# Kernel tuning notes

Hardware: AMD Instinct MI355X
Metric: run time of the kernel (lower is better)

## Reference

```python
import jax, jax.numpy as jnp
import numpy as np

N = 50000
E = 800000
IN_DIM = 128
HID = 128
OUT_DIM = 128
H = 16
D = OUT_DIM // H  # head_dim = 8
EF = 4
RF = 20
KV_IN = 2 * IN_DIM + EF + RF  # 280
EPS = 1e-5


def _layernorm(x, w, b):
    mu = jnp.mean(x, axis=-1, keepdims=True)
    var = jnp.var(x, axis=-1, keepdims=True)
    return (x - mu) * jax.lax.rsqrt(var + EPS) * w + b


def _mlp(x, W1, b1, ln_w, ln_b, W2, b2):
    # Linear -> LayerNorm -> ReLU -> Linear (num_layer=2, norm=True)
    hdn = x @ W1 + b1
    hdn = jax.nn.relu(_layernorm(hdn, ln_w, ln_b))
    return hdn @ W2 + b2


def _lin_init(key, fan_in, fan_out):
    k1, k2 = jax.random.split(key)
    s = 1.0 / np.sqrt(fan_in)
    W = jax.random.uniform(k1, (fan_in, fan_out), jnp.float32, -s, s)
    b = jax.random.uniform(k2, (fan_out,), jnp.float32, -s, s)
    return W, b


def _mlp_params(key, in_dim, hid, out_dim):
    k1, k2 = jax.random.split(key)
    W1, b1 = _lin_init(k1, in_dim, hid)
    W2, b2 = _lin_init(k2, hid, out_dim)
    return W1, b1, jnp.ones((hid,), jnp.float32), jnp.zeros((hid,), jnp.float32), W2, b2


def setup_inputs() -> dict:
    key = jax.random.key(0)
    ks = jax.random.split(key, 10)
    h = jax.random.normal(ks[0], (N, IN_DIM), jnp.float32)
    rel_x = jax.random.normal(ks[1], (E, 3), jnp.float32)
    r_feat = jax.random.normal(ks[2], (E, RF), jnp.float32)
    edge_feat = jax.random.normal(ks[3], (E, EF), jnp.float32)
    edge_index = jax.random.randint(ks[4], (2, E), 0, N, jnp.int64)

    xk = _mlp_params(ks[5], KV_IN, HID, OUT_DIM)
    xv = _mlp_params(ks[6], KV_IN, HID, H)
    xq = _mlp_params(ks[7], IN_DIM, HID, OUT_DIM)
    ew_W, ew_b = _lin_init(ks[8], RF, 1)

    d = {"h": h, "rel_x": rel_x, "r_feat": r_feat, "edge_feat": edge_feat,
         "edge_index": edge_index, "ew_W": ew_W, "ew_b": ew_b}
    for name, p in (("xk", xk), ("xv", xv), ("xq", xq)):
        d[name + "_W1"], d[name + "_b1"], d[name + "_ln_w"], d[name + "_ln_b"], d[name + "_W2"], d[name + "_b2"] = p
    return d


def reference(h, rel_x, r_feat, edge_feat, edge_index,
              ew_W, ew_b,
              xk_W1, xk_b1, xk_ln_w, xk_ln_b, xk_W2, xk_b2,
              xv_W1, xv_b1, xv_ln_w, xv_ln_b, xv_W2, xv_b2,
              xq_W1, xq_b1, xq_ln_w, xq_ln_b, xq_W2, xq_b2):
    src, dst = edge_index[0], edge_index[1]
    hi = h[dst]  # [E, IN_DIM]
    hj = h[src]  # [E, IN_DIM]
    kv_input = jnp.concatenate([edge_feat, r_feat, hi, hj], axis=-1)  # [E, KV_IN]

    k = _mlp(kv_input, xk_W1, xk_b1, xk_ln_w, xk_ln_b, xk_W2, xk_b2).reshape(E, H, D)
    v = _mlp(kv_input, xv_W1, xv_b1, xv_ln_w, xv_ln_b, xv_W2, xv_b2)  # [E, H]
    e_w = jax.nn.sigmoid(r_feat @ ew_W + ew_b)  # [E, 1]
    v = (v * e_w)[:, :, None] * rel_x[:, None, :]  # [E, H, 3]

    q = _mlp(h, xq_W1, xq_b1, xq_ln_w, xq_ln_b, xq_W2, xq_b2).reshape(N, H, D)
    scores = jnp.sum(q[dst] * k, axis=-1) / np.sqrt(D)  # [E, H]

    # scatter_softmax over destination groups
    seg_max = jax.ops.segment_max(scores, dst, num_segments=N)  # [N, H]
    ex = jnp.exp(scores - seg_max[dst])
    denom = jax.ops.segment_sum(ex, dst, num_segments=N)  # [N, H]
    alpha = ex / denom[dst]  # [E, H]

    m = alpha[:, :, None] * v  # [E, H, 3]
    output = jax.ops.segment_sum(m, dst, num_segments=N)  # [N, H, 3]
    return output.mean(axis=1)  # [N, 3]
```

## Files before the change

### kernel.cpp

```cpp
#include <hip/hip_runtime.h>
#include <hip/hip_bf16.h>

#define NN 50000
#define EE 800000
#define ET 32
#define SCB 49

typedef unsigned int u32;
typedef __attribute__((ext_vector_type(8))) short short8;
typedef __attribute__((ext_vector_type(4))) float floatx4;

template<bool BF>
__device__ __forceinline__ float ldf(const void* p, int i){
  if constexpr (BF) return __bfloat162float(((const __hip_bfloat16*)p)[i]);
  else              return ((const float*)p)[i];
}
__device__ __forceinline__ int gidx(const int* ei, int pos, bool i64){
  return i64 ? ei[2*pos] : ei[pos];
}

__device__ __forceinline__ unsigned short f2bf(float f){
  u32 u = __float_as_uint(f);
  u32 r = u + 0x7FFFu + ((u>>16)&1u);
  return (unsigned short)(r>>16);
}
__device__ __forceinline__ float bf2f(unsigned short s){
  return __uint_as_float(((u32)s)<<16);
}

__global__ void k_detect(const u32* lnw, const u32* ei, int* flags){
  if (threadIdx.x == 0){
    flags[0] = (lnw[0] == 0x3F803F80u) ? 1 : 0;
    flags[1] = ((ei[1] | ei[3] | ei[5] | ei[7]) == 0u) ? 1 : 0;
  }
}

__global__ void __launch_bounds__(256)
k_hist(const int* ei, int* cnt, const int* flags){
  int t = blockIdx.x*256 + threadIdx.x;
  if (t >= EE) return;
  bool i64 = flags[1] != 0;
  atomicAdd(&cnt[gidx(ei, EE + t, i64)], 1);
}

__global__ void __launch_bounds__(256)
k_scan1(const int* cnt, int* bsum){
  __shared__ int wsum[4];
  int t=threadIdx.x, lane=t&63, wv=t>>6;
  int i0 = blockIdx.x*1024 + t*4;
  int s=0;
  #pragma unroll
  for(int j=0;j<4;j++){ int i=i0+j; s += (i<NN)?cnt[i]:0; }
  #pragma unroll
  for(int d=1;d<64;d<<=1) s += __shfl_xor(s,d);
  if(lane==0) wsum[wv]=s;
  __syncthreads();
  if(t==0) bsum[blockIdx.x]=wsum[0]+wsum[1]+wsum[2]+wsum[3];
}

__global__ void k_scan2(const int* bsum, int* bexcl, int* off){
  int lane=threadIdx.x;
  int v = (lane<SCB)?bsum[lane]:0;
  int sc=v;
  #pragma unroll
  for(int d=1;d<64;d<<=1){ int u=__shfl_up(sc,d); if(lane>=d) sc+=u; }
  if(lane<SCB) bexcl[lane]=sc-v;
  if(lane==63) off[NN]=sc;
}

__global__ void __launch_bounds__(256)
k_scan3(const int* cnt, const int* bexcl, int* off){
  __shared__ int wsum[4];
  int t=threadIdx.x, lane=t&63, wv=t>>6;
  int i0=blockIdx.x*1024 + t*4;
  int v0=(i0+0<NN)?cnt[i0+0]:0;
  int v1=(i0+1<NN)?cnt[i0+1]:0;
  int v2=(i0+2<NN)?cnt[i0+2]:0;
  int v3=(i0+3<NN)?cnt[i0+3]:0;
  int s=v0+v1+v2+v3;
  int sc=s;
  #pragma unroll
  for(int d=1;d<64;d<<=1){ int u=__shfl_up(sc,d); if(lane>=d) sc+=u; }
  if(lane==63) wsum[wv]=sc;
  __syncthreads();
  int base=bexcl[blockIdx.x];
  for(int k=0;k<wv;k++) base+=wsum[k];
  int excl=base+sc-s;
  if(i0+0<NN) off[i0+0]=excl;
  if(i0+1<NN) off[i0+1]=excl+v0;
  if(i0+2<NN) off[i0+2]=excl+v0+v1;
  if(i0+3<NN) off[i0+3]=excl+v0+v1+v2;
}

template<bool BF>
__device__ void scat_body(const int* ei, bool i64, const int* off, int* cur,
                          const void* rfeat, const void* relx,
                          const void* ewW, const void* ewb,
                          int* dsts, int* srcs, int* eperm,
                          float* relx_s, float* ews){
  int t = blockIdx.x*256 + threadIdx.x;
  if (t >= EE) return;
  int d = gidx(ei, EE + t, i64);
  int pos = off[d] + atomicAdd(&cur[d], 1);
  dsts[pos] = d;
  srcs[pos] = gidx(ei, t, i64);
  eperm[pos] = t;
  float aw = ldf<BF>(ewb, 0);
  #pragma unroll
  for (int j=0;j<20;j++) aw = fmaf(ldf<BF>(rfeat, t*20+j), ldf<BF>(ewW,j), aw);
  ews[pos] = (1.f/(1.f + expf(-aw))) * (1.f/16.f);
  relx_s[pos*3+0] = ldf<BF>(relx, t*3+0);
  relx_s[pos*3+1] = ldf<BF>(relx, t*3+1);
  relx_s[pos*3+2] = ldf<BF>(relx, t*3+2);
}
__global__ void __launch_bounds__(256)
k_scat(const int* ei, const int* off, int* cur,
       const void* rfeat, const void* relx, const void* ewW, const void* ewb,
       int* dsts, int* srcs, int* eperm, float* relx_s, float* ews, const int* flags){
  bool i64 = flags[1] != 0;
  if (flags[0]) scat_body<true >(ei,i64,off,cur,rfeat,relx,ewW,ewb,dsts,srcs,eperm,relx_s,ews);
  else          scat_body<false>(ei,i64,off,cur,rfeat,relx,ewW,ewb,dsts,srcs,eperm,relx_s,ews);
}

__global__ void __launch_bounds__(256)
k_wprep(const void* kW1, const void* vW1, const void* kW2, const void* vW2,
        const void* qW1, const void* qW2,
        unsigned short* w1sh, unsigned short* w1sl,
        unsigned short* w1nh, unsigned short* w1nl,
        unsigned short* w2kh, unsigned short* w2kl,
        unsigned short* w2vh, unsigned short* w2vl,
        unsigned short* w1qh, unsigned short* w1ql,
        unsigned short* w2qh, unsigned short* w2ql, const int* flags){
  int idx = blockIdx.x*256 + threadIdx.x;
  bool bf = flags[0] != 0;
  {
    int c = idx>>7, k = idx&127;
    int row = (c<256) ? (24+k) : (152+k);
    int cc  = c & 127;
    const void* W = ((c&255)<128) ? kW1 : vW1;
    float f = bf ? __bfloat162float(((const __hip_bfloat16*)W)[row*128+cc]) : ((const float*)W)[row*128+cc];
    unsigned short h = f2bf(f); w1nh[idx]=h; w1nl[idx]=f2bf(f - bf2f(h));
  }
  if (idx < 16384){ int c = idx>>7, k = idx&127;
    { float f = bf ? __bfloat162float(((const __hip_bfloat16*)kW2)[k*128+c]) : ((const float*)kW2)[k*128+c];
      unsigned short h = f2bf(f); w2kh[idx]=h; w2kl[idx]=f2bf(f - bf2f(h)); }
    { float f = bf ? __bfloat162float(((const __hip_bfloat16*)qW1)[k*128+c]) : ((const float*)qW1)[k*128+c];
      unsigned short h = f2bf(f); w1qh[idx]=h; w1ql[idx]=f2bf(f - bf2f(h)); }
    { float f = bf ? __bfloat162float(((const __hip_bfloat16*)qW2)[k*128+c]) : ((const float*)qW2)[k*128+c];
      unsigned short h = f2bf(f); w2qh[idx]=h; w2ql[idx]=f2bf(f - bf2f(h)); }
  }
  if (idx < 2048){ int c = idx>>7, k = idx&127;
    float f = bf ? __bfloat162float(((const __hip_bfloat16*)vW2)[k*16+c]) : ((const float*)vW2)[k*16+c];
    unsigned short h = f2bf(f); w2vh[idx]=h; w2vl[idx]=f2bf(f - bf2f(h)); }
  if (idx < 8192){ int c = idx>>5, k = idx&31;
    float f = 0.f;
    if (k < 24){
      if (c < 128) f = bf ? __bfloat162float(((const __hip_bfloat16*)kW1)[k*128+c]) : ((const float*)kW1)[k*128+c];
      else         f = bf ? __bfloat162float(((const __hip_bfloat16*)vW1)[k*128+(c-128)]) : ((const float*)vW1)[k*128+(c-128)];
    }
    unsigned short h = f2bf(f); w1sh[idx]=h; w1sl[idx]=f2bf(f - bf2f(h)); }
}

template<bool BF>
__device__ void nodeq_body(const void* h,
                           const unsigned short* w1nh, const unsigned short* w1nl,
                           const unsigned short* w1qh, const unsigned short* w1ql,
                           const unsigned short* w2qh, const unsigned short* w2ql,
                           const void* qb1, const void* qlnw, const void* qlnb, const void* qb2,
                           float* hkd, float* hks, float* qws,
                           unsigned short* xh, unsigned short* xl,
                           unsigned short* yh, unsigned short* yl,
                           float2 (*lnred)[4]){
  const int t = threadIdx.x;
  const int n0 = blockIdx.x*16;
  const int lane = t&63, w = t>>6;
  const int arow = lane&15, agrp = lane>>4;
  { int nd = t>>4, c8 = (t&15)*8;
    float v[8];
    if constexpr (!BF){
      float4 a = *(const float4*)&((const float*)h)[(n0+nd)*128 + c8];
      float4 b = *(const float4*)&((const float*)h)[(n0+nd)*128 + c8 + 4];
      v[0]=a.x; v[1]=a.y; v[2]=a.z; v[3]=a.w; v[4]=b.x; v[5]=b.y; v[6]=b.z; v[7]=b.w;
    } else {
      short8 raw = *(const short8*)&((const __hip_bfloat16*)h)[(n0+nd)*128 + c8];
      #pragma unroll
      for (int i=0;i<8;i++) v[i] = bf2f((unsigned short)raw[i]);
    }
    short8 hv, lv;
    #pragma unroll
    for (int i=0;i<8;i++){
      unsigned short hh = f2bf(v[i]);
      hv[i] = (short)hh; lv[i] = (short)f2bf(v[i]-bf2f(hh));
    }
    int sidx = (nd*128 + c8) ^ ((nd&7)<<3);
    *(short8*)&xh[sidx] = hv;
    *(short8*)&xl[sidx] = lv;
  }
  __syncthreads();
  { floatx4 acc[8];
    #pragma unroll
    for (int ct=0; ct<8; ct++)
      #pragma unroll
      for (int r=0;r<4;r++) acc[ct][r]=0.f;
    #pragma unroll
    for (int ks=0; ks<4; ks++){
      int aidx = (arow*128 + ks*32 + agrp*8) ^ ((arow&7)<<3);
      short8 Ah = *(const short8*)&xh[aidx];
      short8 Al = *(const short8*)&xl[aidx];
      #pragma unroll
      for (int ct=0; ct<8; ct++){
        int gc = w*128 + ct*16 + arow;
        short8 Bh = *(const short8*)&w1nh[gc*128 + ks*32 + agrp*8];
        short8 Bl = *(const short8*)&w1nl[gc*128 + ks*32 + agrp*8];
        acc[ct] = __builtin_amdgcn_mfma_f32_16x16x32_bf16(Ah, Bh, acc[ct], 0,0,0);
        acc[ct] = __builtin_amdgcn_mfma_f32_16x16x32_bf16(Al, Bh, acc[ct], 0,0,0);
        acc[ct] = __builtin_amdgcn_mfma_f32_16x16x32_bf16(Ah, Bl, acc[ct], 0,0,0);
      }
    }
    #pragma unroll
    for (int ct=0; ct<8; ct++){
      int gc = w*128 + ct*16 + arow;
      float* dst = (gc<256) ? (hkd + (size_t)0) : (hks - 256);
      #pragma unroll
      for (int r=0;r<4;r++){
        int n = n0 + agrp*4 + r;
        dst[(size_t)n*256 + gc] = acc[ct][r];
      }
    }
  }
  floatx4 Cq[2];
  #pragma unroll
  for (int nt=0; nt<2; nt++){
    int col = w*32 + nt*16 + arow;
    float bb = ldf<BF>(qb1, col);
    #pragma unroll
    for (int r=0;r<4;r++) Cq[nt][r] = bb;
  }
  #pragma unroll
  for (int ks=0; ks<4; ks++){
    int aidx = (arow*128 + ks*32 + agrp*8) ^ ((arow&7)<<3);
    short8 Ah = *(const short8*)&xh[aidx];
    short8 Al = *(const short8*)&xl[aidx];
    #pragma unroll
    for (int nt=0; nt<2; nt++){
      int col = w*32 + nt*16 + arow;
      short8 Bh = *(const short8*)&w1qh[col*128 + ks*32 + agrp*8];
      short8 Bl = *(const short8*)&w1ql[col*128 + ks*32 + agrp*8];
      Cq[nt] = __builtin_amdgcn_mfma_f32_16x16x32_bf16(Ah, Bh, Cq[nt], 0,0,0);
      Cq[nt] = __builtin_amdgcn_mfma_f32_16x16x32_bf16(Al, Bh, Cq[nt], 0,0,0);
      Cq[nt] = __builtin_amdgcn_mfma_f32_16x16x32_bf16(Ah, Bl, Cq[nt], 0,0,0);
    }
  }
  { float s1[4], s2[4];
    #pragma unroll
    for (int r=0;r<4;r++){ s1[r]=0.f; s2[r]=0.f; }
    #pragma unroll
    for (int nt=0; nt<2; nt++)
      #pragma unroll
      for (int r=0;r<4;r++){ float v=Cq[nt][r]; s1[r]+=v; s2[r]=fmaf(v,v,s2[r]); }
    #pragma unroll
    for (int d=1; d<16; d<<=1){
      #pragma unroll
      for (int r=0;r<4;r++){ s1[r]+=__shfl_xor(s1[r],d); s2[r]+=__shfl_xor(s2[r],d); }
    }
    if (arow==0){
      #pragma unroll
      for (int r=0;r<4;r++) lnred[agrp*4+r][w] = make_float2(s1[r], s2[r]);
    }
  }
  __syncthreads();
  float mu[4], rs[4];
  #pragma unroll
  for (int r=0;r<4;r++){
    int row = agrp*4+r;
    float s=0.f, q=0.f;
    #pragma unroll
    for (int k=0;k<4;k++){ float2 p=lnred[row][k]; s+=p.x; q+=p.y; }
    float m = s*(1.f/128.f);
    mu[r]=m; rs[r]=rsqrtf(q*(1.f/128.f) - m*m + 1e-5f);
  }
  #pragma unroll
  for (int nt=0; nt<2; nt++){
    int col = w*32 + nt*16 + arow;
    float lw = ldf<BF>(qlnw, col), lb = ldf<BF>(qlnb, col);
    #pragma unroll
    for (int r=0;r<4;r++){
      int row = agrp*4+r;
      float v = fmaxf((Cq[nt][r]-mu[r])*rs[r]*lw + lb, 0.f);
      unsigned short hh = f2bf(v);
      int idx = (row*128 + col) ^ ((row&7)<<3);
      yh[idx] = hh;
      yl[idx] = f2bf(v - bf2f(hh));
    }
  }
  __syncthreads();
  floatx4 Co[2];
  #pragma unroll
  for (int nt=0; nt<2; nt++){
    int col = w*32 + nt*16 + arow;
    float bb = ldf<BF>(qb2, col);
    #pragma unroll
    for (int r=0;r<4;r++) Co[nt][r] = bb;
  }
  #pragma unroll
  for (int ks=0; ks<4; ks++){
    int aidx = (arow*128 + ks*32 + agrp*8) ^ ((arow&7)<<3);
    short8 Ah = *(const short8*)&yh[aidx];
    short8 Al = *(const short8*)&yl[aidx];
    #pragma unroll
    for (int nt=0; nt<2; nt++){
      int col = w*32 + nt*16 + arow;
      short8 Bh = *(const short8*)&w2qh[col*128 + ks*32 + agrp*8];
      short8 Bl = *(const short8*)&w2ql[col*128 + ks*32 + agrp*8];
      Co[nt] = __builtin_amdgcn_mfma_f32_16x16x32_bf16(Ah, Bh, Co[nt], 0,0,0);
      Co[nt] = __builtin_amdgcn_mfma_f32_16x16x32_bf16(Al, Bh, Co[nt], 0,0,0);
      Co[nt] = __builtin_amdgcn_mfma_f32_16x16x32_bf16(Ah, Bl, Co[nt], 0,0,0);
    }
  }
  #pragma unroll
  for (int nt=0; nt<2; nt++){
    int col = w*32 + nt*16 + arow;
    #pragma unroll
    for (int r=0;r<4;r++){
      int n = n0 + agrp*4 + r;
      qws[(size_t)n*128 + col] = Co[nt][r];
    }
  }
}
__global__ void __launch_bounds__(256)
k_nodeq(const void* h,
        const unsigned short* w1nh, const unsigned short* w1nl,
        const unsigned short* w1qh, const unsigned short* w1ql,
        const unsigned short* w2qh, const unsigned short* w2ql,
        const void* qb1, const void* qlnw, const void* qlnb, const void* qb2,
        float* hkd, float* hks, float* qws, const int* flags){
  __shared__ unsigned short xh[16*128];
  __shared__ unsigned short xl[16*128];
  __shared__ unsigned short yh[16*128];
  __shared__ unsigned short yl[16*128];
  __shared__ float2 lnred[16][4];
  if (flags[0]) nodeq_body<true >(h,w1nh,w1nl,w1qh,w1ql,w2qh,w2ql,qb1,qlnw,qlnb,qb2,hkd,hks,qws,xh,xl,yh,yl,lnred);
  else          nodeq_body<false>(h,w1nh,w1nl,w1qh,w1ql,w2qh,w2ql,qb1,qlnw,qlnb,qb2,hkd,hks,qws,xh,xl,yh,yl,lnred);
}

template<bool BF>
__device__ void edge_body(const void* rfeat, const void* efeat,
                          const int* dsts, const int* srcs, const int* eperm,
                          const void* kb1, const void* vb1,
                          const void* klnw, const void* klnb,
                          const void* vlnw, const void* vlnb,
                          const void* kb2, const void* vb2,
                          const unsigned short* w1sh, const unsigned short* w1sl,
                          const unsigned short* w2kh, const unsigned short* w2kl,
                          const unsigned short* w2vh, const unsigned short* w2vl,
                          const float* hkd, const float* hks, const float* qws,
                          const float* ews, float* scw, float* vsw,
                          unsigned short* ahi, unsigned short* sfh,
                          int* dste, int* srce, float* ewv,
                          float2 (*lnred)[4], float* sc_lds){
  const int t  = threadIdx.x;
  const int e0 = blockIdx.x*ET;
  const int lane = t&63, w = t>>6;
  const int arow = lane&15, agrp = lane>>4;

  if (t < ET)             dste[t]    = dsts[e0+t];
  else if (t < 2*ET)      srce[t-ET] = srcs[e0+(t-ET)];
  else if (t < 3*ET)      ewv[t-2*ET] = ews[e0+(t-2*ET)];
  #pragma unroll
  for (int it=0; it<4; it++){
    int id = it*256+t; int e = id>>5, j = id&31;
    int ge = eperm[e0+e];
    float f = (j<4) ? ldf<BF>(efeat, ge*4+j)
            : (j<24 ? ldf<BF>(rfeat, ge*20+(j-4)) : 0.f);
    sfh[e*40+j] = f2bf(f);
  }
  __syncthreads();

  const int wcol = w*64 + arow;
  float b1c[4];
  #pragma unroll
  for (int nt=0; nt<4; nt++){ int col = wcol + nt*16;
    b1c[nt] = (col<128) ? ldf<BF>(kb1,col) : ldf<BF>(vb1,col-128); }
  floatx4 C[2][4];
  #pragma unroll
  for (int g=0; g<2; g++){
    #pragma unroll
    for (int r=0;r<4;r++){
      int e = g*16 + agrp*4 + r;
      const float* bd = hkd + (u32)dste[e]*256u + wcol;
      const float* bs = hks + (u32)srce[e]*256u + wcol;
      #pragma unroll
      for (int nt=0; nt<4; nt++)
        C[g][nt][r] = bd[nt*16] + bs[nt*16] + b1c[nt];
    }
  }
  #pragma unroll
  for (int g=0; g<2; g++){
    short8 Ah = *(const short8*)&sfh[(g*16+arow)*40 + agrp*8];
    #pragma unroll
    for (int nt=0; nt<4; nt++){
      const int col = wcol + nt*16;
      short8 Bh = *(const short8*)&w1sh[col*32 + agrp*8];
      short8 Bl = *(const short8*)&w1sl[col*32 + agrp*8];
      C[g][nt] = __builtin_amdgcn_mfma_f32_16x16x32_bf16(Ah, Bh, C[g][nt], 0,0,0);
      C[g][nt] = __builtin_amdgcn_mfma_f32_16x16x32_bf16(Ah, Bl, C[g][nt], 0,0,0);
    }
  }
  #pragma unroll
  for (int g=0; g<2; g++){
    float s1[4], s2[4];
    #pragma unroll
    for (int r=0;r<4;r++){ s1[r]=0.f; s2[r]=0.f; }
    #pragma unroll
    for (int nt=0; nt<4; nt++)
      #pragma unroll
      for (int r=0;r<4;r++){ float v=C[g][nt][r]; s1[r]+=v; s2[r]=fmaf(v,v,s2[r]); }
    #pragma unroll
    for (int d=1; d<16; d<<=1){
      #pragma unroll
      for (int r=0;r<4;r++){ s1[r]+=__shfl_xor(s1[r],d); s2[r]+=__shfl_xor(s2[r],d); }
    }
    if (arow==0){
      #pragma unroll
      for (int r=0;r<4;r++) lnred[g*16+agrp*4+r][w] = make_float2(s1[r], s2[r]);
    }
  }
  __syncthreads();
  float mu[2][4], rs[2][4];
  { int b = w>>1;
    #pragma unroll
    for (int g=0; g<2; g++)
      #pragma unroll
      for (int r=0;r<4;r++){
        int row = g*16+agrp*4+r;
        float2 p0 = lnred[row][2*b], p1 = lnred[row][2*b+1];
        float s = p0.x+p1.x, q = p0.y+p1.y;
        float m = s*(1.f/128.f);
        mu[g][r]=m; rs[g][r]=rsqrtf(q*(1.f/128.f) - m*m + 1e-5f);
      }
  }
  #pragma unroll
  for (int nt=0; nt<4; nt++){
    const int col = wcol + nt*16;
    const bool kb = (col<128); const int cc = kb?col:col-128;
    float lw = kb?ldf<BF>(klnw,cc):ldf<BF>(vlnw,cc);
    float lb = kb?ldf<BF>(klnb,cc):ldf<BF>(vlnb,cc);
    #pragma unroll
    for (int g=0; g<2; g++){
      #pragma unroll
      for (int r=0;r<4;r++){
        int row = g*16+agrp*4+r;
        float v = (C[g][nt][r]-mu[g][r])*rs[g][r]*lw + lb;
        v = fmaxf(v, 0.f);
        int idx = (row*256 + col) ^ ((row&7)<<3);
        ahi[idx] = f2bf(v);
      }
    }
  }
  __syncthreads();

  const int c0 = (2*w+0)*16 + arow;
  const int c1 = (2*w+1)*16 + arow;
  floatx4 Ck[2][2], Cv;
  { float b0=ldf<BF>(kb2,c0), b1v=ldf<BF>(kb2,c1);
    #pragma unroll
    for (int g=0;g<2;g++)
      #pragma unroll
      for (int r=0;r<4;r++){ Ck[g][0][r]=b0; Ck[g][1][r]=b1v; } }
  const bool dov = (w&1);
  const int  gv  = w>>1;
  if (dov){ float bv=ldf<BF>(vb2,arow);
    #pragma unroll
    for (int r=0;r<4;r++) Cv[r]=bv; }
  #pragma unroll
  for (int ks=0; ks<4; ks++){
    short8 B0h = *(const short8*)&w2kh[c0*128 + ks*32 + agrp*8];
    short8 B0l = *(const short8*)&w2kl[c0*128 + ks*32 + agrp*8];
    short8 B1h = *(const short8*)&w2kh[c1*128 + ks*32 + agrp*8];
    short8 B1l = *(const short8*)&w2kl[c1*128 + ks*32 + agrp*8];
    #pragma unroll
    for (int g=0; g<2; g++){
      int aidx = ((g*16+arow)*256 + ks*32 + agrp*8) ^ ((arow&7)<<3);
      short8 Ah = *(const short8*)&ahi[aidx];
      Ck[g][0] = __builtin_amdgcn_mfma_f32_16x16x32_bf16(Ah, B0h, Ck[g][0], 0,0,0);
      Ck[g][0] = __builtin_amdgcn_mfma_f32_16x16x32_bf16(Ah, B0l, Ck[g][0], 0,0,0);
      Ck[g][1] = __builtin_amdgcn_mfma_f32_16x16x32_bf16(Ah, B1h, Ck[g][1], 0,0,0);
      Ck[g][1] = __builtin_amdgcn_mfma_f32_16x16x32_bf16(Ah, B1l, Ck[g][1], 0,0,0);
    }
    if (dov){
      int avidx = ((gv*16+arow)*256 + 128 + ks*32 + agrp*8) ^ ((arow&7)<<3);
      short8 Avh = *(const short8*)&ahi[avidx];
      short8 Bvh = *(const short8*)&w2vh[arow*128 + ks*32 + agrp*8];
      short8 Bvl = *(const short8*)&w2vl[arow*128 + ks*32 + agrp*8];
      Cv = __builtin_amdgcn_mfma_f32_16x16x32_bf16(Avh, Bvh, Cv, 0,0,0);
      Cv = __builtin_amdgcn_mfma_f32_16x16x32_bf16(Avh, Bvl, Cv, 0,0,0);
    }
  }
  if (dov){
    #pragma unroll
    for (int r=0;r<4;r++){
      int row = gv*16 + agrp*4 + r;
      vsw[(size_t)(e0+row)*16 + arow] = Cv[r]*ewv[row];
    }
  }
  #pragma unroll
  for (int g=0; g<2; g++){
    float p0[4], p1[4];
    #pragma unroll
    for (int r=0;r<4;r++){
      int e = g*16 + agrp*4 + r;
      const float* qr = qws + (u32)dste[e]*128u;
      p0[r] = qr[c0]*Ck[g][0][r];
      p1[r] = qr[c1]*Ck[g][1][r];
    }
    #pragma unroll
    for (int d=1; d<8; d<<=1){
      #pragma unroll
      for (int r=0;r<4;r++){ p0[r]+=__shfl_xor(p0[r],d); p1[r]+=__shfl_xor(p1[r],d); }
    }
    int j = arow&7;
    float val = (j<4) ? ((j&2)?((j&1)?p0[3]:p0[2]):((j&1)?p0[1]:p0[0]))
                      : ((j&2)?((j&1)?p1[3]:p1[2]):((j&1)?p1[1]:p1[0]));
    int e  = g*16 + agrp*4 + (j&3);
    int hh = (j<4) ? (4*w + (arow>>3)) : (4*w + 2 + (arow>>3));
    sc_lds[e*17 + hh] = val*0.35355339059327373f;
  }
  __syncthreads();
  #pragma unroll
  for (int u=0; u<2; u++){
    int idx = u*256 + t;
    scw[(size_t)e0*16 + idx] = sc_lds[(idx>>4)*17 + (idx&15)];
  }
}
__global__ void __launch_bounds__(256)
k_edge(const void* rfeat, const void* efeat,
       const int* dsts, const int* srcs, const int* eperm,
       const void* kb1, const void* vb1,
       const void* klnw, const void* klnb, const void* vlnw, const void* vlnb,
       const void* kb2, const void* vb2,
       const unsigned short* w1sh, const unsigned short* w1sl,
       const unsigned short* w2kh, const unsigned short* w2kl,
       const unsigned short* w2vh, const unsigned short* w2vl,
       const float* hkd, const float* hks, const float* qws,
       const float* ews, float* scw, float* vsw, const int* flags){
  __shared__ unsigned short ahi[ET*256];
  __shared__ unsigned short sfh[ET*40];
  __shared__ int   dste[ET], srce[ET];
  __shared__ float ewv[ET];
  __shared__ float2 lnred[ET][4];
  __shared__ float sc_lds[ET*17];
  if (flags[0]) edge_body<true >(rfeat,efeat,dsts,srcs,eperm,kb1,vb1,klnw,klnb,vlnw,vlnb,kb2,vb2,
                                 w1sh,w1sl,w2kh,w2kl,w2vh,w2vl,hkd,hks,qws,ews,scw,vsw,
                                 ahi,sfh,dste,srce,ewv,lnred,sc_lds);
  else          edge_body<false>(rfeat,efeat,dsts,srcs,eperm,kb1,vb1,klnw,klnb,vlnw,vlnb,kb2,vb2,
                                 w1sh,w1sl,w2kh,w2kl,w2vh,w2vl,hkd,hks,qws,ews,scw,vsw,
                                 ahi,sfh,dste,srce,ewv,lnred,sc_lds);
}

template<bool BF>
__device__ void soft_body(const int* off, const float* relx_s,
                          const float* scw, const float* vsw, void* dout){
  const int t=threadIdx.x, lane=t&63, wv=t>>6;
  const int n = blockIdx.x*4 + wv;
  const int lo=off[n], hi=off[n+1];
  if (lo>=hi){
    if (lane<3){
      if constexpr (BF) ((__hip_bfloat16*)dout)[n*3+lane]=__float2bfloat16(0.f);
      else              ((float*)dout)[n*3+lane]=0.f;
    }
    return;
  }
  const int h=lane&15, es=lane>>4;
  float m=-3.4e38f;
  for (int p=lo+es; p<hi; p+=4) m = fmaxf(m, scw[(size_t)p*16+h]);
  m = fmaxf(m, __shfl_xor(m,16));
  m = fmaxf(m, __shfl_xor(m,32));
  float den=0.f, t0=0.f, t1=0.f, t2=0.f;
  for (int p=lo+es; p<hi; p+=4){
    float ex = expf(scw[(size_t)p*16+h]-m);
    den += ex;
    float a = ex * vsw[(size_t)p*16+h];
    float r0=relx_s[p*3+0], r1=relx_s[p*3+1], r2=relx_s[p*3+2];
    t0 = fmaf(a,r0,t0); t1 = fmaf(a,r1,t1); t2 = fmaf(a,r2,t2);
  }
  den += __shfl_xor(den,16);
  den += __shfl_xor(den,32);
  float id = 1.f/den;
  t0*=id; t1*=id; t2*=id;
  #pragma unroll
  for (int d=1; d<64; d<<=1){
    t0+=__shfl_xor(t0,d); t1+=__shfl_xor(t1,d); t2+=__shfl_xor(t2,d);
  }
  if (lane==0){
    if constexpr (BF){
      ((__hip_bfloat16*)dout)[n*3+0]=__float2bfloat16(t0);
      ((__hip_bfloat16*)dout)[n*3+1]=__float2bfloat16(t1);
      ((__hip_bfloat16*)dout)[n*3+2]=__float2bfloat16(t2);
    } else {
      ((float*)dout)[n*3+0]=t0;
      ((float*)dout)[n*3+1]=t1;
      ((float*)dout)[n*3+2]=t2;
    }
  }
}
__global__ void __launch_bounds__(256)
k_soft(const int* off, const float* relx_s,
       const float* scw, const float* vsw, void* dout, const int* flags){
  if (flags[0]) soft_body<true >(off,relx_s,scw,vsw,dout);
  else          soft_body<false>(off,relx_s,scw,vsw,dout);
}

extern "C" void kernel_launch(void* const* d_in, const int* in_sizes, int n_in,
                              void* d_out, int out_size, void* d_ws, size_t ws_size,
                              hipStream_t stream){
  const void* h     = d_in[0];
  const void* relx  = d_in[1];
  const void* rfeat = d_in[2];
  const void* efeat = d_in[3];
  const int*  ei    = (const int*)d_in[4];
  const void* ewW   = d_in[5];
  const void* ewb   = d_in[6];
  const void* kW1 = d_in[7],  *kb1 = d_in[8],  *klnw = d_in[9],  *klnb = d_in[10], *kW2 = d_in[11], *kb2 = d_in[12];
  const void* vW1 = d_in[13], *vb1 = d_in[14], *vlnw = d_in[15], *vlnb = d_in[16], *vW2 = d_in[17], *vb2 = d_in[18];
  const void* qW1 = d_in[19], *qb1 = d_in[20], *qlnw = d_in[21], *qlnb = d_in[22], *qW2 = d_in[23], *qb2 = d_in[24];

  float* qws = (float*)d_ws;
  float* hkd = qws + (size_t)NN*128;
  float* hks = hkd + (size_t)NN*256;
  float* scw = hks + (size_t)NN*256;
  float* vsw = scw + (size_t)EE*16;
  float* relx_s = vsw + (size_t)EE*16;
  float* ews = relx_s + (size_t)EE*3;
  int*   cnt = (int*)(ews + EE);
  int*   cur = cnt + NN;
  int*   off = cur + NN;
  int*  dsts = off + NN + 64;
  int*  srcs = dsts + EE;
  int* eperm = srcs + EE;
  unsigned short* w1sh = (unsigned short*)(eperm + EE);
  unsigned short* w1sl = w1sh + 8192;
  unsigned short* w1nh = w1sl + 8192;
  unsigned short* w1nl = w1nh + 65536;
  unsigned short* w2kh = w1nl + 65536;
  unsigned short* w2kl = w2kh + 16384;
  unsigned short* w2vh = w2kl + 16384;
  unsigned short* w2vl = w2vh + 2048;
  unsigned short* w1qh = w2vl + 2048;
  unsigned short* w1ql = w1qh + 16384;
  unsigned short* w2qh = w1ql + 16384;
  unsigned short* w2ql = w2qh + 16384;
  int* bsum  = (int*)(w2ql + 16384);
  int* bexcl = bsum + 64;
  int* flags = bexcl + 64;

  hipMemsetAsync(cnt, 0, (size_t)2*NN*sizeof(int), stream);
  k_detect<<<1, 64, 0, stream>>>((const u32*)klnw, (const u32*)ei, flags);
  k_hist<<<(EE+255)/256, 256, 0, stream>>>(ei, cnt, flags);
  k_scan1<<<SCB, 256, 0, stream>>>(cnt, bsum);
  k_scan2<<<1, 64, 0, stream>>>(bsum, bexcl, off);
  k_scan3<<<SCB, 256, 0, stream>>>(cnt, bexcl, off);
  k_scat<<<(EE+255)/256, 256, 0, stream>>>(ei, off, cur, rfeat, relx, ewW, ewb,
                                           dsts, srcs, eperm, relx_s, ews, flags);
  k_wprep<<<256, 256, 0, stream>>>(kW1, vW1, kW2, vW2, qW1, qW2,
                                   w1sh, w1sl, w1nh, w1nl, w2kh, w2kl, w2vh, w2vl,
                                   w1qh, w1ql, w2qh, w2ql, flags);
  k_nodeq<<<NN/16, 256, 0, stream>>>(h, w1nh, w1nl, w1qh, w1ql, w2qh, w2ql,
                                     qb1, qlnw, qlnb, qb2, hkd, hks, qws, flags);
  k_edge<<<EE/ET, 256, 0, stream>>>(rfeat, efeat, dsts, srcs, eperm,
                                    kb1, vb1, klnw, klnb, vlnw, vlnb, kb2, vb2,
                                    w1sh, w1sl, w2kh, w2kl, w2vh, w2vl,
                                    hkd, hks, qws, ews, scw, vsw, flags);
  k_soft<<<(NN+3)/4, 256, 0, stream>>>(off, relx_s, scw, vsw, d_out, flags);
}
```

Before: 835.9 us.

## Pack per-edge metadata into one blob and permute node tables for vector gathers

Per-edge scatter outputs (dst, src, permutation, edge weight, rel_x) are packed into one 32-byte record per sorted edge, replacing five separate arrays. The per-node hidden tables and q are written in a permuted column order so the edge kernel can gather each row with float4/float2 loads instead of strided scalar loads. The first-layer bias is folded into the node-side table. This cuts the number of gather transactions in the edge kernel, in exchange for a larger padded record and more complex index mapping.

```diff
diff --git a/kernel.cpp b/kernel.cpp
--- a/kernel.cpp
+++ b/kernel.cpp
@@ -95,31 +95,30 @@
 template<bool BF>
 __device__ void scat_body(const int* ei, bool i64, const int* off, int* cur,
                           const void* rfeat, const void* relx,
-                          const void* ewW, const void* ewb,
-                          int* dsts, int* srcs, int* eperm,
-                          float* relx_s, float* ews){
+                          const void* ewW, const void* ewb, float* blob){
   int t = blockIdx.x*256 + threadIdx.x;
   if (t >= EE) return;
   int d = gidx(ei, EE + t, i64);
   int pos = off[d] + atomicAdd(&cur[d], 1);
-  dsts[pos] = d;
-  srcs[pos] = gidx(ei, t, i64);
-  eperm[pos] = t;
   float aw = ldf<BF>(ewb, 0);
   #pragma unroll
   for (int j=0;j<20;j++) aw = fmaf(ldf<BF>(rfeat, t*20+j), ldf<BF>(ewW,j), aw);
-  ews[pos] = (1.f/(1.f + expf(-aw))) * (1.f/16.f);
-  relx_s[pos*3+0] = ldf<BF>(relx, t*3+0);
-  relx_s[pos*3+1] = ldf<BF>(relx, t*3+1);
-  relx_s[pos*3+2] = ldf<BF>(relx, t*3+2);
+  int4 a; a.x=d; a.y=gidx(ei, t, i64); a.z=t; a.w=0;
+  float4 b;
+  b.x = (1.f/(1.f + expf(-aw))) * (1.f/16.f);
+  b.y = ldf<BF>(relx, t*3+0);
+  b.z = ldf<BF>(relx, t*3+1);
+  b.w = ldf<BF>(relx, t*3+2);
+  ((int4*)blob)[2*(size_t)pos]   = a;
+  ((float4*)blob)[2*(size_t)pos+1] = b;
 }
 __global__ void __launch_bounds__(256)
 k_scat(const int* ei, const int* off, int* cur,
        const void* rfeat, const void* relx, const void* ewW, const void* ewb,
-       int* dsts, int* srcs, int* eperm, float* relx_s, float* ews, const int* flags){
+       float* blob, const int* flags){
   bool i64 = flags[1] != 0;
-  if (flags[0]) scat_body<true >(ei,i64,off,cur,rfeat,relx,ewW,ewb,dsts,srcs,eperm,relx_s,ews);
-  else          scat_body<false>(ei,i64,off,cur,rfeat,relx,ewW,ewb,dsts,srcs,eperm,relx_s,ews);
+  if (flags[0]) scat_body<true >(ei,i64,off,cur,rfeat,relx,ewW,ewb,blob);
+  else          scat_body<false>(ei,i64,off,cur,rfeat,relx,ewW,ewb,blob);
 }
 
 __global__ void __launch_bounds__(256)
@@ -166,6 +165,7 @@
                            const unsigned short* w1nh, const unsigned short* w1nl,
                            const unsigned short* w1qh, const unsigned short* w1ql,
                            const unsigned short* w2qh, const unsigned short* w2ql,
+                           const void* kb1, const void* vb1,
                            const void* qb1, const void* qlnw, const void* qlnb, const void* qb2,
                            float* hkd, float* hks, float* qws,
                            unsigned short* xh, unsigned short* xl,
@@ -217,15 +217,24 @@
         acc[ct] = __builtin_amdgcn_mfma_f32_16x16x32_bf16(Ah, Bl, acc[ct], 0,0,0);
       }
     }
-    #pragma unroll
-    for (int ct=0; ct<8; ct++){
-      int gc = w*128 + ct*16 + arow;
-      float* dst = (gc<256) ? (hkd + (size_t)0) : (hks - 256);
-      #pragma unroll
-      for (int r=0;r<4;r++){
-        int n = n0 + agrp*4 + r;
-        dst[(size_t)n*256 + gc] = acc[ct][r];
+    if (w < 2){
+      #pragma unroll
+      for (int ct=0; ct<8; ct++){
+        int gc = w*128 + ct*16 + arow;
+        float bb = (gc<128) ? ldf<BF>(kb1,gc) : ldf<BF>(vb1,gc-128);
+        #pragma unroll
+        for (int r=0;r<4;r++) acc[ct][r] += bb;
       }
+    }
+    float* base = (w<2) ? hkd : hks;
+    const int boff = (w&1)*8;
+    #pragma unroll
+    for (int r=0;r<4;r++){
+      int n = n0 + agrp*4 + r;
+      float4 lo4 = make_float4(acc[0][r],acc[1][r],acc[2][r],acc[3][r]);
+      float4 hi4 = make_float4(acc[4][r],acc[5][r],acc[6][r],acc[7][r]);
+      *(float4*)&base[(size_t)n*256 + arow*16 + boff]     = lo4;
+      *(float4*)&base[(size_t)n*256 + arow*16 + boff + 4] = hi4;
     }
   }
   floatx4 Cq[2];
@@ -318,13 +327,9 @@
     }
   }
   #pragma unroll
-  for (int nt=0; nt<2; nt++){
-    int col = w*32 + nt*16 + arow;
-    #pragma unroll
-    for (int r=0;r<4;r++){
-      int n = n0 + agrp*4 + r;
-      qws[(size_t)n*128 + col] = Co[nt][r];
-    }
+  for (int r=0;r<4;r++){
+    int n = n0 + agrp*4 + r;
+    *(float2*)&qws[(size_t)n*128 + arow*8 + w*2] = make_float2(Co[0][r], Co[1][r]);
   }
 }
 __global__ void __launch_bounds__(256)
@@ -332,6 +337,7 @@
         const unsigned short* w1nh, const unsigned short* w1nl,
         const unsigned short* w1qh, const unsigned short* w1ql,
         const unsigned short* w2qh, const unsigned short* w2ql,
+        const void* kb1, const void* vb1,
         const void* qb1, const void* qlnw, const void* qlnb, const void* qb2,
         float* hkd, float* hks, float* qws, const int* flags){
   __shared__ unsigned short xh[16*128];
@@ -339,14 +345,12 @@
   __shared__ unsigned short yh[16*128];
   __shared__ unsigned short yl[16*128];
   __shared__ float2 lnred[16][4];
-  if (flags[0]) nodeq_body<true >(h,w1nh,w1nl,w1qh,w1ql,w2qh,w2ql,qb1,qlnw,qlnb,qb2,hkd,hks,qws,xh,xl,yh,yl,lnred);
-  else          nodeq_body<false>(h,w1nh,w1nl,w1qh,w1ql,w2qh,w2ql,qb1,qlnw,qlnb,qb2,hkd,hks,qws,xh,xl,yh,yl,lnred);
+  if (flags[0]) nodeq_body<true >(h,w1nh,w1nl,w1qh,w1ql,w2qh,w2ql,kb1,vb1,qb1,qlnw,qlnb,qb2,hkd,hks,qws,xh,xl,yh,yl,lnred);
+  else          nodeq_body<false>(h,w1nh,w1nl,w1qh,w1ql,w2qh,w2ql,kb1,vb1,qb1,qlnw,qlnb,qb2,hkd,hks,qws,xh,xl,yh,yl,lnred);
 }
 
 template<bool BF>
-__device__ void edge_body(const void* rfeat, const void* efeat,
-                          const int* dsts, const int* srcs, const int* eperm,
-                          const void* kb1, const void* vb1,
+__device__ void edge_body(const void* rfeat, const void* efeat, const float* blob,
                           const void* klnw, const void* klnb,
                           const void* vlnw, const void* vlnb,
                           const void* kb2, const void* vb2,
@@ -354,7 +358,7 @@
                           const unsigned short* w2kh, const unsigned short* w2kl,
                           const unsigned short* w2vh, const unsigned short* w2vl,
                           const float* hkd, const float* hks, const float* qws,
-                          const float* ews, float* scw, float* vsw,
+                          float* scw, float* vsw,
                           unsigned short* ahi, unsigned short* sfh,
                           int* dste, int* srce, float* ewv,
                           float2 (*lnred)[4], float* sc_lds){
@@ -362,14 +366,15 @@
   const int e0 = blockIdx.x*ET;
   const int lane = t&63, w = t>>6;
   const int arow = lane&15, agrp = lane>>4;
-
-  if (t < ET)             dste[t]    = dsts[e0+t];
-  else if (t < 2*ET)      srce[t-ET] = srcs[e0+(t-ET)];
-  else if (t < 3*ET)      ewv[t-2*ET] = ews[e0+(t-2*ET)];
+  const int* bi = (const int*)blob;
+
+  if (t < ET)             dste[t]     = bi[(size_t)(e0+t)*8 + 0];
+  else if (t < 2*ET)      srce[t-ET]  = bi[(size_t)(e0+t-ET)*8 + 1];
+  else if (t < 3*ET)      ewv[t-2*ET] = blob[(size_t)(e0+t-2*ET)*8 + 4];
   #pragma unroll
   for (int it=0; it<4; it++){
     int id = it*256+t; int e = id>>5, j = id&31;
-    int ge = eperm[e0+e];
+    int ge = bi[(size_t)(e0+e)*8 + 2];
     float f = (j<4) ? ldf<BF>(efeat, ge*4+j)
             : (j<24 ? ldf<BF>(rfeat, ge*20+(j-4)) : 0.f);
     sfh[e*40+j] = f2bf(f);
@@ -377,21 +382,17 @@
   __syncthreads();
 
   const int wcol = w*64 + arow;
-  float b1c[4];
-  #pragma unroll
-  for (int nt=0; nt<4; nt++){ int col = wcol + nt*16;
-    b1c[nt] = (col<128) ? ldf<BF>(kb1,col) : ldf<BF>(vb1,col-128); }
+  const int pbase = arow*16 + w*4;
   floatx4 C[2][4];
   #pragma unroll
   for (int g=0; g<2; g++){
     #pragma unroll
     for (int r=0;r<4;r++){
       int e = g*16 + agrp*4 + r;
-      const float* bd = hkd + (u32)dste[e]*256u + wcol;
-      const float* bs = hks + (u32)srce[e]*256u + wcol;
-      #pragma unroll
-      for (int nt=0; nt<4; nt++)
-        C[g][nt][r] = bd[nt*16] + bs[nt*16] + b1c[nt];
+      float4 gd = *(const float4*)&hkd[(size_t)(u32)dste[e]*256u + pbase];
+      float4 gs = *(const float4*)&hks[(size_t)(u32)srce[e]*256u + pbase];
+      C[g][0][r] = gd.x+gs.x; C[g][1][r] = gd.y+gs.y;
+      C[g][2][r] = gd.z+gs.z; C[g][3][r] = gd.w+gs.w;
     }
   }
   #pragma unroll
@@ -509,9 +510,9 @@
     #pragma unroll
     for (int r=0;r<4;r++){
       int e = g*16 + agrp*4 + r;
-      const float* qr = qws + (u32)dste[e]*128u;
-      p0[r] = qr[c0]*Ck[g][0][r];
-      p1[r] = qr[c1]*Ck[g][1][r];
+      float2 q2 = *(const float2*)&qws[(size_t)(u32)dste[e]*128u + arow*8 + 2*w];
+      p0[r] = q2.x*Ck[g][0][r];
+      p1[r] = q2.y*Ck[g][1][r];
     }
     #pragma unroll
     for (int d=1; d<8; d<<=1){
@@ -533,32 +534,30 @@
   }
 }
 __global__ void __launch_bounds__(256)
-k_edge(const void* rfeat, const void* efeat,
-       const int* dsts, const int* srcs, const int* eperm,
-       const void* kb1, const void* vb1,
+k_edge(const void* rfeat, const void* efeat, const float* blob,
        const void* klnw, const void* klnb, const void* vlnw, const void* vlnb,
        const void* kb2, const void* vb2,
        const unsigned short* w1sh, const unsigned short* w1sl,
        const unsigned short* w2kh, const unsigned short* w2kl,
        const unsigned short* w2vh, const unsigned short* w2vl,
        const float* hkd, const float* hks, const float* qws,
-       const float* ews, float* scw, float* vsw, const int* flags){
+       float* scw, float* vsw, const int* flags){
   __shared__ unsigned short ahi[ET*256];
   __shared__ unsigned short sfh[ET*40];
   __shared__ int   dste[ET], srce[ET];
   __shared__ float ewv[ET];
   __shared__ float2 lnred[ET][4];
   __shared__ float sc_lds[ET*17];
-  if (flags[0]) edge_body<true >(rfeat,efeat,dsts,srcs,eperm,kb1,vb1,klnw,klnb,vlnw,vlnb,kb2,vb2,
-                                 w1sh,w1sl,w2kh,w2kl,w2vh,w2vl,hkd,hks,qws,ews,scw,vsw,
+  if (flags[0]) edge_body<true >(rfeat,efeat,blob,klnw,klnb,vlnw,vlnb,kb2,vb2,
+                                 w1sh,w1sl,w2kh,w2kl,w2vh,w2vl,hkd,hks,qws,scw,vsw,
                                  ahi,sfh,dste,srce,ewv,lnred,sc_lds);
-  else          edge_body<false>(rfeat,efeat,dsts,srcs,eperm,kb1,vb1,klnw,klnb,vlnw,vlnb,kb2,vb2,
-                                 w1sh,w1sl,w2kh,w2kl,w2vh,w2vl,hkd,hks,qws,ews,scw,vsw,
+  else          edge_body<false>(rfeat,efeat,blob,klnw,klnb,vlnw,vlnb,kb2,vb2,
+                                 w1sh,w1sl,w2kh,w2kl,w2vh,w2vl,hkd,hks,qws,scw,vsw,
                                  ahi,sfh,dste,srce,ewv,lnred,sc_lds);
 }
 
 template<bool BF>
-__device__ void soft_body(const int* off, const float* relx_s,
+__device__ void soft_body(const int* off, const float* blob,
                           const float* scw, const float* vsw, void* dout){
   const int t=threadIdx.x, lane=t&63, wv=t>>6;
   const int n = blockIdx.x*4 + wv;
@@ -580,8 +579,8 @@
     float ex = expf(scw[(size_t)p*16+h]-m);
     den += ex;
     float a = ex * vsw[(size_t)p*16+h];
-    float r0=relx_s[p*3+0], r1=relx_s[p*3+1], r2=relx_s[p*3+2];
-    t0 = fmaf(a,r0,t0); t1 = fmaf(a,r1,t1); t2 = fmaf(a,r2,t2);
+    float4 rx = ((const float4*)blob)[2*(size_t)p+1];
+    t0 = fmaf(a,rx.y,t0); t1 = fmaf(a,rx.z,t1); t2 = fmaf(a,rx.w,t2);
   }
   den += __shfl_xor(den,16);
   den += __shfl_xor(den,32);
@@ -604,10 +603,10 @@
   }
 }
 __global__ void __launch_bounds__(256)
-k_soft(const int* off, const float* relx_s,
+k_soft(const int* off, const float* blob,
        const float* scw, const float* vsw, void* dout, const int* flags){
-  if (flags[0]) soft_body<true >(off,relx_s,scw,vsw,dout);
-  else          soft_body<false>(off,relx_s,scw,vsw,dout);
+  if (flags[0]) soft_body<true >(off,blob,scw,vsw,dout);
+  else          soft_body<false>(off,blob,scw,vsw,dout);
 }
 
 extern "C" void kernel_launch(void* const* d_in, const int* in_sizes, int n_in,
@@ -629,15 +628,11 @@
   float* hks = hkd + (size_t)NN*256;
   float* scw = hks + (size_t)NN*256;
   float* vsw = scw + (size_t)EE*16;
-  float* relx_s = vsw + (size_t)EE*16;
-  float* ews = relx_s + (size_t)EE*3;
-  int*   cnt = (int*)(ews + EE);
+  float* blob = vsw + (size_t)EE*16;
+  int*   cnt = (int*)(blob + (size_t)EE*8);
   int*   cur = cnt + NN;
   int*   off = cur + NN;
-  int*  dsts = off + NN + 64;
-  int*  srcs = dsts + EE;
-  int* eperm = srcs + EE;
-  unsigned short* w1sh = (unsigned short*)(eperm + EE);
+  unsigned short* w1sh = (unsigned short*)(off + NN + 64);
   unsigned short* w1sl = w1sh + 8192;
   unsigned short* w1nh = w1sl + 8192;
   unsigned short* w1nl = w1nh + 65536;
@@ -660,15 +655,16 @@
   k_scan2<<<1, 64, 0, stream>>>(bsum, bexcl, off);
   k_scan3<<<SCB, 256, 0, stream>>>(cnt, bexcl, off);
   k_scat<<<(EE+255)/256, 256, 0, stream>>>(ei, off, cur, rfeat, relx, ewW, ewb,
-                                           dsts, srcs, eperm, relx_s, ews, flags);
+                                           blob, flags);
   k_wprep<<<256, 256, 0, stream>>>(kW1, vW1, kW2, vW2, qW1, qW2,
                                    w1sh, w1sl, w1nh, w1nl, w2kh, w2kl, w2vh, w2vl,
                                    w1qh, w1ql, w2qh, w2ql, flags);
   k_nodeq<<<NN/16, 256, 0, stream>>>(h, w1nh, w1nl, w1qh, w1ql, w2qh, w2ql,
-                                     qb1, qlnw, qlnb, qb2, hkd, hks, qws, flags);
-  k_edge<<<EE/ET, 256, 0, stream>>>(rfeat, efeat, dsts, srcs, eperm,
-                                    kb1, vb1, klnw, klnb, vlnw, vlnb, kb2, vb2,
+                                     kb1, vb1, qb1, qlnw, qlnb, qb2,
+                                     hkd, hks, qws, flags);
+  k_edge<<<EE/ET, 256, 0, stream>>>(rfeat, efeat, blob,
+                                    klnw, klnb, vlnw, vlnb, kb2, vb2,
                                     w1sh, w1sl, w2kh, w2kl, w2vh, w2vl,
-                                    hkd, hks, qws, ews, scw, vsw, flags);
-  k_soft<<<(NN+3)/4, 256, 0, stream>>>(off, relx_s, scw, vsw, d_out, flags);
-}
+                                    hkd, hks, qws, scw, vsw, flags);
+  k_soft<<<(NN+3)/4, 256, 0, stream>>>(off, blob, scw, vsw, d_out, flags);
+}
```

Result: faster. 804.1 us (-3.8%).
